# Kernel tuning notes

Hardware: AMD Instinct MI355X
Metric: run time of the kernel (lower is better)

The kernel has to match this reference:

```python
import jax, jax.numpy as jnp
import numpy as np

NEG = float(-2**32 + 1)  # padding value used by the original module
N_HEADS = 4


def setup_inputs() -> dict:
    key = jax.random.key(0)
    ks = jax.random.split(key, 12)
    B, L, H = 16, 200, 256
    queries = jax.random.normal(ks[0], (B, L, H), jnp.float32)
    keys = jax.random.normal(ks[1], (B, L, H), jnp.float32)
    time_mask = jax.random.randint(ks[2], (B, L), 0, 2) == 1
    attn_mask = jnp.triu(jnp.ones((L, L), dtype=bool), k=1)  # causal: True = masked
    time_matrix_K = jax.random.normal(ks[3], (B, L, L, H), jnp.float32) * 0.1
    time_matrix_V = jax.random.normal(ks[4], (B, L, L, H), jnp.float32) * 0.1
    abs_pos_K = jax.random.normal(ks[5], (B, L, H), jnp.float32)
    abs_pos_V = jax.random.normal(ks[6], (B, L, H), jnp.float32)
    s = 1.0 / np.sqrt(H)
    Wq = jax.random.normal(ks[7], (H, H), jnp.float32) * s
    Wk = jax.random.normal(ks[8], (H, H), jnp.float32) * s
    Wv = jax.random.normal(ks[9], (H, H), jnp.float32) * s
    bq = jnp.zeros((H,), jnp.float32)
    bk = jnp.zeros((H,), jnp.float32)
    bv = jnp.zeros((H,), jnp.float32)
    return dict(queries=queries, keys=keys, time_mask=time_mask, attn_mask=attn_mask,
                time_matrix_K=time_matrix_K, time_matrix_V=time_matrix_V,
                abs_pos_K=abs_pos_K, abs_pos_V=abs_pos_V,
                Wq=Wq, bq=bq, Wk=Wk, bk=bk, Wv=Wv, bv=bv)


def reference(queries, keys, time_mask, attn_mask, time_matrix_K, time_matrix_V,
              abs_pos_K, abs_pos_V, Wq, bq, Wk, bk, Wv, bv):
    B, L, H = queries.shape
    h = N_HEADS
    d = H // h
    # linear projections
    Q = (queries @ Wq.T + bq).reshape(B, L, h, d)
    K = (keys @ Wk.T + bk).reshape(B, L, h, d)
    V = (keys @ Wv.T + bv).reshape(B, L, h, d)
    posK = abs_pos_K.reshape(B, L, h, d)
    posV = abs_pos_V.reshape(B, L, h, d)
    tmK = time_matrix_K.reshape(B, L, L, h, d)
    tmV = time_matrix_V.reshape(B, L, L, h, d)
    # attention scores: content + absolute-position bias + per-row time bias
    scores = jnp.einsum('blhd,bmhd->bhlm', Q, K)
    scores += jnp.einsum('blhd,bmhd->bhlm', Q, posK)
    scores += jnp.einsum('blmhd,blhd->bhlm', tmK, Q)
    scores = scores / jnp.sqrt(jnp.asarray(d, scores.dtype))
    # time_mask masks query rows; attn_mask is causal [L,L]
    mask = time_mask[:, None, :, None] | attn_mask[None, None, :, :]  # [B,1,L,L]
    scores = jnp.where(mask, NEG, scores)
    A = jax.nn.softmax(scores, axis=-1)  # [B,h,L,L]; dropout_rate=0 -> identity
    out = jnp.einsum('bhlm,bmhd->blhd', A, V)
    out += jnp.einsum('bhlm,bmhd->blhd', A, posV)
    out += jnp.einsum('bhlm,blmhd->blhd', A, tmV)
    return out.reshape(B, L, H)
```

## Files before the change

### kernel.cpp

```cpp
#include <hip/hip_runtime.h>
#include <math.h>

#define LQ 200
#define HDIM 256
#define NROW 3200
#define NBLK 1024

template <int CTRL>
__device__ __forceinline__ float dpp_add_step(float x) {
    int y = __builtin_amdgcn_update_dpp(0, __float_as_int(x), CTRL, 0xF, 0xF, true);
    return x + __int_as_float(y);
}
__device__ __forceinline__ float reduce16(float x) {
    x = dpp_add_step<0xB1>(x);
    x = dpp_add_step<0x4E>(x);
    x = dpp_add_step<0x141>(x);
    x = dpp_add_step<0x140>(x);
    return x;
}

__global__ __launch_bounds__(256) void proj_kernel(
    const float* __restrict__ queries, const float* __restrict__ keys,
    const float* __restrict__ posK, const float* __restrict__ posV,
    const float* __restrict__ Wq, const float* __restrict__ bq,
    const float* __restrict__ Wk, const float* __restrict__ bk,
    const float* __restrict__ Wv, const float* __restrict__ bv,
    float* __restrict__ Qp, float* __restrict__ Ksum, float* __restrict__ Vsum)
{
    __shared__ float qrow[8][HDIM];
    __shared__ float krow[8][HDIM];
    const int t = threadIdx.x;
    const int blk = blockIdx.x;
    const size_t base = (size_t)blk * 8 * HDIM;

    #pragma unroll
    for (int i = 0; i < 2; ++i) {
        int idx = i * 1024 + t * 4;
        *(float4*)&qrow[0][idx] = *(const float4*)&queries[base + idx];
        *(float4*)&krow[0][idx] = *(const float4*)&keys[base + idx];
    }
    __syncthreads();

    float accQ[8], accK[8], accV[8];
    #pragma unroll
    for (int r = 0; r < 8; ++r) { accQ[r] = 0.f; accK[r] = 0.f; accV[r] = 0.f; }

    const float4* wqp = (const float4*)&Wq[t * HDIM];
    const float4* wkp = (const float4*)&Wk[t * HDIM];
    const float4* wvp = (const float4*)&Wv[t * HDIM];

    for (int k4 = 0; k4 < HDIM / 4; ++k4) {
        float4 wq = wqp[k4], wk = wkp[k4], wv = wvp[k4];
        #pragma unroll
        for (int r = 0; r < 8; ++r) {
            float4 qv = *(const float4*)&qrow[r][k4 * 4];
            float4 kv = *(const float4*)&krow[r][k4 * 4];
            accQ[r] += qv.x * wq.x + qv.y * wq.y + qv.z * wq.z + qv.w * wq.w;
            accK[r] += kv.x * wk.x + kv.y * wk.y + kv.z * wk.z + kv.w * wk.w;
            accV[r] += kv.x * wv.x + kv.y * wv.y + kv.z * wv.z + kv.w * wv.w;
        }
    }

    const float bqv = bq[t], bkv = bk[t], bvv = bv[t];
    #pragma unroll
    for (int r = 0; r < 8; ++r) {
        size_t row = (size_t)blk * 8 + r;
        Qp[row * HDIM + t]   = (accQ[r] + bqv) * 0.125f;
        Ksum[row * HDIM + t] = accK[r] + bkv + posK[row * HDIM + t];
        Vsum[row * HDIM + t] = accV[r] + bvv + posV[row * HDIM + t];
    }
}

__global__ __launch_bounds__(256) void scan_kernel(
    const int* __restrict__ tmask, int* __restrict__ Upre)
{
    __shared__ int sh[256];
    const int t = threadIdx.x;
    int carry = 0;
    for (int chunk = 0; chunk < 13; ++chunk) {
        const int idx = chunk * 256 + t;
        int cv = 0;
        if (idx < NROW) {
            const int l = idx % LQ;
            cv = (tmask[idx] != 0) ? (LQ / 8) : ((l + 4) >> 2);
        }
        sh[t] = cv;
        __syncthreads();
        for (int off = 1; off < 256; off <<= 1) {
            int v = (t >= off) ? sh[t - off] : 0;
            __syncthreads();
            sh[t] += v;
            __syncthreads();
        }
        if (idx < NROW) Upre[idx] = carry + sh[t] - cv;
        carry += sh[255];
        __syncthreads();
    }
    if (t == 0) Upre[NROW] = carry;
}

__global__ __launch_bounds__(256, 4) void attn_pass(
    const float* __restrict__ Qp, const float* __restrict__ Ksum,
    const float* __restrict__ Vsum, const float* __restrict__ tmK,
    const float* __restrict__ tmV, const int* __restrict__ tmask,
    const int* __restrict__ Upre, float* __restrict__ pacc,
    float* __restrict__ pS)
{
    const int t = threadIdx.x;
    const int w = t >> 6;
    const int ln = t & 63;
    const int h = ln >> 4;
    const int c = ln * 4;
    const int bid0 = blockIdx.x;
    const int bid = (bid0 & 7) * (NBLK / 8) + (bid0 >> 3);
    const int U = Upre[NROW];
    const long s0 = ((long)bid * U) / NBLK;
    const long s1 = ((long)(bid + 1) * U) / NBLK;
    if (s0 >= s1) return;

    int lo = 0, hi = NROW;
    while (lo + 1 < hi) {
        const int mid = (lo + hi) >> 1;
        if (Upre[mid] <= (int)s0) lo = mid; else hi = mid;
    }
    int row = lo;
    long u = s0;

    while (u < s1) {
        const int rbase = Upre[row];
        const int rcnt  = Upre[row + 1] - rbase;
        const int ku0 = (int)(u - rbase);
        int ku1 = rcnt;
        { const long rem = (s1 - u) + ku0; if (rem < (long)ku1) ku1 = (int)rem; }

        const int b = row / LQ;
        const int l = row - b * LQ;
        const float* tV = tmV + (size_t)row * (LQ * HDIM);
        const float* VS = Vsum + (size_t)b * (LQ * HDIM);

        float4 acc = {0.f, 0.f, 0.f, 0.f};
        float S = 0.f;

        if (tmask[row] != 0) {
            for (int k = ku0; k < ku1; ++k) {
                const int m = 8 * k + w;
                const size_t o0 = (size_t)m * HDIM + c;
                const size_t o1 = o0 + 4 * HDIM;
                const float4 a0 = *(const float4*)&tV[o0];
                const float4 b0 = *(const float4*)&VS[o0];
                const float4 a1 = *(const float4*)&tV[o1];
                const float4 b1 = *(const float4*)&VS[o1];
                acc.x += (a0.x + b0.x) + (a1.x + b1.x);
                acc.y += (a0.y + b0.y) + (a1.y + b1.y);
                acc.z += (a0.z + b0.z) + (a1.z + b1.z);
                acc.w += (a0.w + b0.w) + (a1.w + b1.w);
                S += 2.f;
            }
        } else {
            const float* tK = tmK + (size_t)row * (LQ * HDIM);
            const float* KS = Ksum + (size_t)b * (LQ * HDIM);
            const float4 Q4 = *(const float4*)&Qp[(size_t)row * HDIM + c];
            for (int k = ku0; k < ku1; ++k) {
                const int m = 4 * k + w;
                if (m <= l) {
                    const size_t o = (size_t)m * HDIM + c;
                    const float4 k1v = *(const float4*)&tK[o];
                    const float4 k2v = *(const float4*)&KS[o];
                    float p = Q4.x * (k1v.x + k2v.x) + Q4.y * (k1v.y + k2v.y)
                            + Q4.z * (k1v.z + k2v.z) + Q4.w * (k1v.w + k2v.w);
                    p = reduce16(p);
                    const float e = __expf(p);
                    const float4 v1 = *(const float4*)&tV[o];
                    const float4 v2 = *(const float4*)&VS[o];
                    acc.x += e * (v1.x + v2.x);
                    acc.y += e * (v1.y + v2.y);
                    acc.z += e * (v1.z + v2.z);
                    acc.w += e * (v1.w + v2.w);
                    S += e;
                }
            }
        }

        float* pr = pacc + (size_t)row * HDIM + c;
        atomicAdd(pr + 0, acc.x);
        atomicAdd(pr + 1, acc.y);
        atomicAdd(pr + 2, acc.z);
        atomicAdd(pr + 3, acc.w);
        if ((ln & 15) == 0) atomicAdd(&pS[row * 4 + h], S);

        u += (ku1 - ku0);
        ++row;
    }
}

__global__ __launch_bounds__(256) void combine_kernel(
    const float* __restrict__ pacc, const float* __restrict__ pS,
    float* __restrict__ out)
{
    const int row = blockIdx.x;
    const int t = threadIdx.x;
    out[(size_t)row * HDIM + t] =
        pacc[(size_t)row * HDIM + t] / pS[row * 4 + (t >> 6)];
}

extern "C" void kernel_launch(void* const* d_in, const int* in_sizes, int n_in,
                              void* d_out, int out_size, void* d_ws, size_t ws_size,
                              hipStream_t stream) {
    const float* queries = (const float*)d_in[0];
    const float* keys    = (const float*)d_in[1];
    const int*   tmask   = (const int*)d_in[2];
    const float* tmK  = (const float*)d_in[4];
    const float* tmV  = (const float*)d_in[5];
    const float* posK = (const float*)d_in[6];
    const float* posV = (const float*)d_in[7];
    const float* Wq = (const float*)d_in[8];
    const float* bq = (const float*)d_in[9];
    const float* Wk = (const float*)d_in[10];
    const float* bk = (const float*)d_in[11];
    const float* Wv = (const float*)d_in[12];
    const float* bv = (const float*)d_in[13];

    float* ws   = (float*)d_ws;
    float* Qp   = ws;
    float* Ksum = ws + 819200;
    float* Vsum = ws + 2 * 819200;
    float* pacc = ws + 3 * 819200;
    float* pS   = ws + 4 * 819200;
    int*   Upre = (int*)(ws + 4 * 819200 + 12800);
    float* out  = (float*)d_out;

    hipMemsetAsync(pacc, 0, (size_t)(819200 + 12800) * sizeof(float), stream);

    hipLaunchKernelGGL(proj_kernel, dim3(400), dim3(256), 0, stream,
                       queries, keys, posK, posV, Wq, bq, Wk, bk, Wv, bv,
                       Qp, Ksum, Vsum);
    hipLaunchKernelGGL(scan_kernel, dim3(1), dim3(256), 0, stream,
                       tmask, Upre);
    hipLaunchKernelGGL(attn_pass, dim3(NBLK), dim3(256), 0, stream,
                       Qp, Ksum, Vsum, tmK, tmV, tmask, Upre, pacc, pS);
    hipLaunchKernelGGL(combine_kernel, dim3(NROW), dim3(256), 0, stream,
                       pacc, pS, out);
}
```

Before: 271.3 us.

## Replace atomic accumulation with per-unit partial buffers and table-driven sweep

Builds a work-unit lookup table so each block can sweep units strided across the grid instead of binary-searching a contiguous range. Each unit's four wavefront partials are reduced through double-buffered shared memory and written to a dedicated partial slot, which removes the global atomics and the zeroing memset. The combine kernel then sums all partial slots belonging to each row. In exchange it writes and rereads a large partial buffer, adds a block barrier per unit, and greatly enlarges the required workspace.

```diff
diff --git a/kernel.cpp b/kernel.cpp
--- a/kernel.cpp
+++ b/kernel.cpp
@@ -4,7 +4,8 @@
 #define LQ 200
 #define HDIM 256
 #define NROW 3200
-#define NBLK 1024
+#define NBLK 2048
+#define MAXU 160000
 
 template <int CTRL>
 __device__ __forceinline__ float dpp_add_step(float x) {
@@ -99,108 +100,117 @@
     if (t == 0) Upre[NROW] = carry;
 }
 
-__global__ __launch_bounds__(256, 4) void attn_pass(
+__global__ __launch_bounds__(256) void fill_kernel(
+    const int* __restrict__ Upre, int* __restrict__ table)
+{
+    const int row = blockIdx.x * 256 + threadIdx.x;
+    if (row >= NROW) return;
+    const int u0 = Upre[row], u1 = Upre[row + 1];
+    for (int u = u0; u < u1; ++u) table[u] = (row << 6) | (u - u0);
+}
+
+__global__ __launch_bounds__(256) void attn_sweep(
     const float* __restrict__ Qp, const float* __restrict__ Ksum,
     const float* __restrict__ Vsum, const float* __restrict__ tmK,
     const float* __restrict__ tmV, const int* __restrict__ tmask,
-    const int* __restrict__ Upre, float* __restrict__ pacc,
-    float* __restrict__ pS)
-{
+    const int* __restrict__ Upre, const int* __restrict__ table,
+    float* __restrict__ pacc, float* __restrict__ pS)
+{
+    __shared__ float outp[2][4][HDIM];
+    __shared__ float Ssh[2][4][4];
+
     const int t = threadIdx.x;
     const int w = t >> 6;
     const int ln = t & 63;
     const int h = ln >> 4;
     const int c = ln * 4;
-    const int bid0 = blockIdx.x;
-    const int bid = (bid0 & 7) * (NBLK / 8) + (bid0 >> 3);
+    const int k = blockIdx.x;
     const int U = Upre[NROW];
-    const long s0 = ((long)bid * U) / NBLK;
-    const long s1 = ((long)(bid + 1) * U) / NBLK;
-    if (s0 >= s1) return;
-
-    int lo = 0, hi = NROW;
-    while (lo + 1 < hi) {
-        const int mid = (lo + hi) >> 1;
-        if (Upre[mid] <= (int)s0) lo = mid; else hi = mid;
-    }
-    int row = lo;
-    long u = s0;
-
-    while (u < s1) {
-        const int rbase = Upre[row];
-        const int rcnt  = Upre[row + 1] - rbase;
-        const int ku0 = (int)(u - rbase);
-        int ku1 = rcnt;
-        { const long rem = (s1 - u) + ku0; if (rem < (long)ku1) ku1 = (int)rem; }
-
-        const int b = row / LQ;
-        const int l = row - b * LQ;
-        const float* tV = tmV + (size_t)row * (LQ * HDIM);
-        const float* VS = Vsum + (size_t)b * (LQ * HDIM);
-
-        float4 acc = {0.f, 0.f, 0.f, 0.f};
-        float S = 0.f;
-
-        if (tmask[row] != 0) {
-            for (int k = ku0; k < ku1; ++k) {
-                const int m = 8 * k + w;
-                const size_t o0 = (size_t)m * HDIM + c;
-                const size_t o1 = o0 + 4 * HDIM;
-                const float4 a0 = *(const float4*)&tV[o0];
-                const float4 b0 = *(const float4*)&VS[o0];
-                const float4 a1 = *(const float4*)&tV[o1];
-                const float4 b1 = *(const float4*)&VS[o1];
-                acc.x += (a0.x + b0.x) + (a1.x + b1.x);
-                acc.y += (a0.y + b0.y) + (a1.y + b1.y);
-                acc.z += (a0.z + b0.z) + (a1.z + b1.z);
-                acc.w += (a0.w + b0.w) + (a1.w + b1.w);
-                S += 2.f;
+    const int nstep = (U + 2 * NBLK - 1) / (2 * NBLK);
+    const size_t rowsz = (size_t)LQ * HDIM;
+
+    int pb = 0;
+    for (int j = 0; j < nstep; ++j) {
+        #pragma unroll
+        for (int c2 = 0; c2 < 2; ++c2) {
+            const int u = (j * NBLK + k) * 2 + c2;
+            if (u < U) {
+                const int desc = table[u];
+                const int row = desc >> 6;
+                const int ku = desc & 63;
+                const int b = row / LQ;
+                const int l = row - b * LQ;
+                const float* tV = tmV + (size_t)row * rowsz;
+                const float* VS = Vsum + (size_t)b * rowsz;
+
+                float4 acc = {0.f, 0.f, 0.f, 0.f};
+                float S = 0.f;
+
+                if (tmask[row] != 0) {
+                    const size_t o0 = (size_t)(8 * ku + w) * HDIM + c;
+                    const size_t o1 = o0 + 4 * HDIM;
+                    const float4 a0 = *(const float4*)&tV[o0];
+                    const float4 b0 = *(const float4*)&VS[o0];
+                    const float4 a1 = *(const float4*)&tV[o1];
+                    const float4 b1 = *(const float4*)&VS[o1];
+                    acc.x = (a0.x + b0.x) + (a1.x + b1.x);
+                    acc.y = (a0.y + b0.y) + (a1.y + b1.y);
+                    acc.z = (a0.z + b0.z) + (a1.z + b1.z);
+                    acc.w = (a0.w + b0.w) + (a1.w + b1.w);
+                    S = 2.f;
+                } else {
+                    const int m = 4 * ku + w;
+                    if (m <= l) {
+                        const size_t o = (size_t)m * HDIM + c;
+                        const float* tK = tmK + (size_t)row * rowsz;
+                        const float* KS = Ksum + (size_t)b * rowsz;
+                        const float4 k1 = *(const float4*)&tK[o];
+                        const float4 k2 = *(const float4*)&KS[o];
+                        const float4 v1 = *(const float4*)&tV[o];
+                        const float4 v2 = *(const float4*)&VS[o];
+                        const float4 Q4 =
+                            *(const float4*)&Qp[(size_t)row * HDIM + c];
+                        float p = Q4.x * (k1.x + k2.x) + Q4.y * (k1.y + k2.y)
+                                + Q4.z * (k1.z + k2.z) + Q4.w * (k1.w + k2.w);
+                        p = reduce16(p);
+                        const float e = __expf(p);
+                        acc.x = e * (v1.x + v2.x);
+                        acc.y = e * (v1.y + v2.y);
+                        acc.z = e * (v1.z + v2.z);
+                        acc.w = e * (v1.w + v2.w);
+                        S = e;
+                    }
+                }
+                *(float4*)&outp[pb][w][c] = acc;
+                if ((ln & 15) == 0) Ssh[pb][w][h] = S;
             }
-        } else {
-            const float* tK = tmK + (size_t)row * (LQ * HDIM);
-            const float* KS = Ksum + (size_t)b * (LQ * HDIM);
-            const float4 Q4 = *(const float4*)&Qp[(size_t)row * HDIM + c];
-            for (int k = ku0; k < ku1; ++k) {
-                const int m = 4 * k + w;
-                if (m <= l) {
-                    const size_t o = (size_t)m * HDIM + c;
-                    const float4 k1v = *(const float4*)&tK[o];
-                    const float4 k2v = *(const float4*)&KS[o];
-                    float p = Q4.x * (k1v.x + k2v.x) + Q4.y * (k1v.y + k2v.y)
-                            + Q4.z * (k1v.z + k2v.z) + Q4.w * (k1v.w + k2v.w);
-                    p = reduce16(p);
-                    const float e = __expf(p);
-                    const float4 v1 = *(const float4*)&tV[o];
-                    const float4 v2 = *(const float4*)&VS[o];
-                    acc.x += e * (v1.x + v2.x);
-                    acc.y += e * (v1.y + v2.y);
-                    acc.z += e * (v1.z + v2.z);
-                    acc.w += e * (v1.w + v2.w);
-                    S += e;
-                }
+            __syncthreads();
+            if (u < U) {
+                const float a = outp[pb][0][t] + outp[pb][1][t]
+                              + outp[pb][2][t] + outp[pb][3][t];
+                pacc[(size_t)u * HDIM + t] = a;
+                if (t < 4)
+                    pS[(size_t)u * 4 + t] = Ssh[pb][0][t] + Ssh[pb][1][t]
+                                          + Ssh[pb][2][t] + Ssh[pb][3][t];
             }
-        }
-
-        float* pr = pacc + (size_t)row * HDIM + c;
-        atomicAdd(pr + 0, acc.x);
-        atomicAdd(pr + 1, acc.y);
-        atomicAdd(pr + 2, acc.z);
-        atomicAdd(pr + 3, acc.w);
-        if ((ln & 15) == 0) atomicAdd(&pS[row * 4 + h], S);
-
-        u += (ku1 - ku0);
-        ++row;
+            pb ^= 1;
+        }
     }
 }
 
 __global__ __launch_bounds__(256) void combine_kernel(
-    const float* __restrict__ pacc, const float* __restrict__ pS,
-    float* __restrict__ out)
+    const int* __restrict__ Upre, const float* __restrict__ pacc,
+    const float* __restrict__ pS, float* __restrict__ out)
 {
     const int row = blockIdx.x;
     const int t = threadIdx.x;
-    out[(size_t)row * HDIM + t] =
-        pacc[(size_t)row * HDIM + t] / pS[row * 4 + (t >> 6)];
+    const int u0 = Upre[row], u1 = Upre[row + 1];
+    float a = 0.f, S = 0.f;
+    for (int u = u0; u < u1; ++u) {
+        a += pacc[(size_t)u * HDIM + t];
+        S += pS[(size_t)u * 4 + (t >> 6)];
+    }
+    out[(size_t)row * HDIM + t] = a / S;
 }
 
 extern "C" void kernel_launch(void* const* d_in, const int* in_sizes, int n_in,
@@ -225,19 +235,20 @@
     float* Ksum = ws + 819200;
     float* Vsum = ws + 2 * 819200;
     float* pacc = ws + 3 * 819200;
-    float* pS   = ws + 4 * 819200;
-    int*   Upre = (int*)(ws + 4 * 819200 + 12800);
+    float* pS   = pacc + (size_t)MAXU * HDIM;
+    int*   Upre = (int*)(pS + (size_t)MAXU * 4);
+    int*   table = Upre + 3204;
     float* out  = (float*)d_out;
-
-    hipMemsetAsync(pacc, 0, (size_t)(819200 + 12800) * sizeof(float), stream);
 
     hipLaunchKernelGGL(proj_kernel, dim3(400), dim3(256), 0, stream,
                        queries, keys, posK, posV, Wq, bq, Wk, bk, Wv, bv,
                        Qp, Ksum, Vsum);
     hipLaunchKernelGGL(scan_kernel, dim3(1), dim3(256), 0, stream,
                        tmask, Upre);
-    hipLaunchKernelGGL(attn_pass, dim3(NBLK), dim3(256), 0, stream,
-                       Qp, Ksum, Vsum, tmK, tmV, tmask, Upre, pacc, pS);
+    hipLaunchKernelGGL(fill_kernel, dim3((NROW + 255) / 256), dim3(256), 0,
+                       stream, Upre, table);
+    hipLaunchKernelGGL(attn_sweep, dim3(NBLK), dim3(256), 0, stream,
+                       Qp, Ksum, Vsum, tmK, tmV, tmask, Upre, table, pacc, pS);
     hipLaunchKernelGGL(combine_kernel, dim3(NROW), dim3(256), 0, stream,
-                       pacc, pS, out);
-}
+                       Upre, pacc, pS, out);
+}
```

New measurement: 308.7 us. +13.8%, slower.
